# Performance work log

Measured on AMD Instinct MI355X. Metric: run time of the kernel, lower is better.

The kernel has to match this reference:

```python
import jax, jax.numpy as jnp
import numpy as np

NUM_HEADS = 32
NUM_KV_HEADS = 8
HEAD_DIM = 128
ROPE_BASE = 10000.0


def rotate_half(x):
    half = x.shape[-1] // 2
    x1, x2 = x[..., :half], x[..., half:]
    return jnp.concatenate((-x2, x1), axis=-1)


def rope_cos_sin(position_ids, head_dim, dtype):
    # inv_freq: [head_dim/2]
    inv_freq = 1.0 / (ROPE_BASE ** (jnp.arange(0, head_dim, 2, dtype=jnp.float32) / head_dim))
    freqs = position_ids.astype(jnp.float32)[..., None] * inv_freq  # [B, S, hd/2]
    emb = jnp.concatenate((freqs, freqs), axis=-1)                  # [B, S, hd]
    # add head axis -> [B, 1, S, hd]
    return jnp.cos(emb)[:, None].astype(dtype), jnp.sin(emb)[:, None].astype(dtype)


def setup_inputs() -> dict:
    key = jax.random.key(0)
    k_x, k_q, k_k, k_v, k_o = jax.random.split(key, 5)
    B, S, H = 1, 2048, 4096
    w_scale = 0.02
    return {
        "hidden_states": jax.random.normal(k_x, (B, S, H), dtype=jnp.float32),
        "position_ids": jnp.broadcast_to(jnp.arange(S, dtype=jnp.int32), (B, S)),
        "Wq": jax.random.normal(k_q, (NUM_HEADS * HEAD_DIM, H), dtype=jnp.float32) * w_scale,
        "Wk": jax.random.normal(k_k, (NUM_KV_HEADS * HEAD_DIM, H), dtype=jnp.float32) * w_scale,
        "Wv": jax.random.normal(k_v, (NUM_KV_HEADS * HEAD_DIM, H), dtype=jnp.float32) * w_scale,
        "Wo": jax.random.normal(k_o, (H, NUM_HEADS * HEAD_DIM), dtype=jnp.float32) * w_scale,
    }


def reference(hidden_states, position_ids, Wq, Wk, Wv, Wo):
    B, S, H = hidden_states.shape
    n_rep = NUM_HEADS // NUM_KV_HEADS

    # projections (torch Linear: y = x @ W.T), reshape to [B, heads, S, hd]
    q = (hidden_states @ Wq.T).reshape(B, S, NUM_HEADS, HEAD_DIM).transpose(0, 2, 1, 3)
    k = (hidden_states @ Wk.T).reshape(B, S, NUM_KV_HEADS, HEAD_DIM).transpose(0, 2, 1, 3)
    v = (hidden_states @ Wv.T).reshape(B, S, NUM_KV_HEADS, HEAD_DIM).transpose(0, 2, 1, 3)

    cos, sin = rope_cos_sin(position_ids, HEAD_DIM, hidden_states.dtype)
    q = q * cos + rotate_half(q) * sin
    k = k * cos + rotate_half(k) * sin

    # repeat_kv: GQA expansion to [B, NUM_HEADS, S, hd]
    k = jnp.repeat(k, n_rep, axis=1)
    v = jnp.repeat(v, n_rep, axis=1)

    scale = 1.0 / jnp.sqrt(jnp.asarray(HEAD_DIM, dtype=hidden_states.dtype))
    scores = jnp.einsum('bhqd,bhkd->bhqk', q, k) * scale  # [B, H, S, S]

    # causal additive mask
    causal = jnp.tril(jnp.ones((S, S), dtype=bool))
    scores = jnp.where(causal[None, None], scores, jnp.finfo(scores.dtype).min)

    probs = jax.nn.softmax(scores, axis=-1)
    attn = jnp.einsum('bhqk,bhkd->bhqd', probs, v)         # [B, H, S, hd]
    attn = attn.transpose(0, 2, 1, 3).reshape(B, S, NUM_HEADS * HEAD_DIM)
    return attn @ Wo.T
```

## Files before the change

kernel.cpp:

```cpp
#include <hip/hip_runtime.h>
#include <hip/hip_bf16.h>
#include <stdint.h>

typedef __bf16 bf16;
typedef __attribute__((ext_vector_type(8))) __bf16 bf16x8;
typedef __attribute__((ext_vector_type(4))) __bf16 bf16x4;
typedef __attribute__((ext_vector_type(4))) float f32x4;
typedef __attribute__((ext_vector_type(16))) float f32x16;
typedef __attribute__((ext_vector_type(4))) unsigned int uint4v;

#define S_LEN 2048
#define HDIM  4096
#define NQH   32
#define NKVH  8
#define DHEAD 128
#define QKVN  6144
#define KOFF  4096
#define VOFF  5120

__device__ __forceinline__ void gload_lds16(const bf16* g, bf16* l) {
  __builtin_amdgcn_global_load_lds(
      (const __attribute__((address_space(1))) unsigned int*)g,
      (__attribute__((address_space(3))) unsigned int*)l, 16, 0, 0);
}

__global__ __launch_bounds__(256) void cvt_f32_bf16(const float* __restrict__ in,
                                                    bf16* __restrict__ out, int n4) {
  int i = blockIdx.x * 256 + threadIdx.x;
  if (i >= n4) return;
  float4 v = ((const float4*)in)[i];
  bf16x4 ov = {(bf16)v.x, (bf16)v.y, (bf16)v.z, (bf16)v.w};
  *(bf16x4*)&out[(size_t)i * 4] = ov;
}

__global__ __launch_bounds__(256) void rope_table(const int* __restrict__ pos,
                                                  float* __restrict__ tab) {
  int idx = blockIdx.x * 256 + threadIdx.x;
  int i = idx & 63, s = idx >> 6;
  float p = (float)pos[s];
  float invf = powf(10000.0f, -(float)i * (1.0f / 64.0f));
  float ang = p * invf;
  tab[idx * 2]     = cosf(ang);
  tab[idx * 2 + 1] = sinf(ang);
}

__global__ __launch_bounds__(256) void rope_apply(bf16* __restrict__ QKV,
                                                  const float* __restrict__ tab) {
  int idx = blockIdx.x * 256 + threadIdx.x;
  int dp = idx & 63;
  int t = idx >> 6;
  int head = t % 40;
  int s = t / 40;
  float c  = tab[(s * 64 + dp) * 2];
  float sn = tab[(s * 64 + dp) * 2 + 1];
  size_t base = (size_t)s * QKVN + head * DHEAD;
  float x0 = (float)QKV[base + dp];
  float x1 = (float)QKV[base + 64 + dp];
  QKV[base + dp]      = (bf16)(x0 * c - x1 * sn);
  QKV[base + 64 + dp] = (bf16)(x1 * c + x0 * sn);
}

__global__ __launch_bounds__(256) void transpose_v(const bf16* __restrict__ QKV,
                                                   bf16* __restrict__ Vt) {
  __shared__ bf16 t[64][72];
  int tid = threadIdx.x;
  int bs = blockIdx.x * 64, bc = blockIdx.y * 64;
  int sl = tid >> 3, cb = (tid & 7) * 8;
#pragma unroll
  for (int ss = 0; ss < 64; ss += 32) {
    int s = sl + ss;
    *(bf16x8*)&t[s][cb] = *(const bf16x8*)&QKV[(size_t)(bs + s) * QKVN + VOFF + bc + cb];
  }
  __syncthreads();
  int cl = tid >> 3, sb = (tid & 7) * 8;
#pragma unroll
  for (int cc = 0; cc < 64; cc += 32) {
    int c = cl + cc;
    bf16x8 v;
#pragma unroll
    for (int k = 0; k < 8; ++k) v[k] = t[sb + k][c];
    *(bf16x8*)&Vt[(size_t)(bc + c) * S_LEN + bs + sb] = v;
  }
}

template <typename OutT>
__global__ __launch_bounds__(256) void gemm_bt(const bf16* __restrict__ A,
                                               const bf16* __restrict__ B,
                                               OutT* __restrict__ C,
                                               int M, int N, int K) {
  __shared__ bf16 At[128 * 64];
  __shared__ bf16 Bt[128 * 64];
  const int tid = threadIdx.x;
  const int w = tid >> 6, lane = tid & 63;
  const int r = lane & 15, g = lane >> 4;
  const int bm = blockIdx.y * 128, bn = blockIdx.x * 128;
  const int wm = (w >> 1) * 64, wn = (w & 1) * 64;
  f32x4 acc[4][4];
#pragma unroll
  for (int i = 0; i < 4; ++i)
#pragma unroll
    for (int j = 0; j < 4; ++j) acc[i][j] = (f32x4){0.f, 0.f, 0.f, 0.f};

  const int chunk0 = w * 256 + lane;

  for (int k0 = 0; k0 < K; k0 += 64) {
#pragma unroll
    for (int i = 0; i < 4; ++i) {
      int chunk = chunk0 + i * 64;
      int row = chunk >> 3, c8 = chunk & 7;
      int cs = ((c8 ^ (row & 7)) << 3) + k0;
      gload_lds16(&A[(size_t)(bm + row) * K + cs], &At[(w * 4 + i) * 512]);
      gload_lds16(&B[(size_t)(bn + row) * K + cs], &Bt[(w * 4 + i) * 512]);
    }
    __syncthreads();
#pragma unroll
    for (int ks = 0; ks < 2; ++ks) {
      bf16x8 af[4], bfr[4];
#pragma unroll
      for (int mi = 0; mi < 4; ++mi) {
        int row = wm + mi * 16 + r;
        af[mi] = *(const bf16x8*)&At[row * 64 + ((((ks << 2) + g) ^ (row & 7)) << 3)];
      }
#pragma unroll
      for (int nj = 0; nj < 4; ++nj) {
        int row = wn + nj * 16 + r;
        bfr[nj] = *(const bf16x8*)&Bt[row * 64 + ((((ks << 2) + g) ^ (row & 7)) << 3)];
      }
#pragma unroll
      for (int mi = 0; mi < 4; ++mi)
#pragma unroll
        for (int nj = 0; nj < 4; ++nj)
          acc[mi][nj] = __builtin_amdgcn_mfma_f32_16x16x32_bf16(af[mi], bfr[nj],
                                                                acc[mi][nj], 0, 0, 0);
    }
    __syncthreads();
  }
#pragma unroll
  for (int mi = 0; mi < 4; ++mi)
#pragma unroll
    for (int nj = 0; nj < 4; ++nj)
#pragma unroll
      for (int j = 0; j < 4; ++j) {
        int row = bm + wm + mi * 16 + g * 4 + j;
        int col = bn + wn + nj * 16 + r;
        C[(size_t)row * N + col] = (OutT)acc[mi][nj][j];
      }
}

__global__ __launch_bounds__(256) void attn_kernel(const bf16* __restrict__ QKV,
                                                   const bf16* __restrict__ Vt,
                                                   bf16* __restrict__ Opart,
                                                   float* __restrict__ Mpart,
                                                   float* __restrict__ Lpart) {
  __shared__ bf16 Kl[2][32 * 128];
  __shared__ bf16 Vl[2][128 * 32];
  const int tid = threadIdx.x;
  const int w = tid >> 6, lane = tid & 63;
  const int l31 = lane & 31, hi = lane >> 5;
  const int bx = blockIdx.x;
  const int kvh = bx & 7;
  const int rem = bx >> 3;
  const int s = rem & 1;
  const int u = rem >> 1;
  const int ua = u & 15, ub = u >> 4;
  const int qblk = (ub & 1) ? ((3 - ub) * 16 + (15 - ua)) : ((3 - ub) * 16 + ua);
  const int h = kvh * 4 + w;
  const int q0 = qblk * 32;
  const int pid = (h * 64 + qblk) * 2 + s;
  const float scale = 0.12751746f;

  const int nt = qblk + 1;
  const int hh = (nt + 1) >> 1;
  const int t0 = s ? hh : 0;
  const int t1 = s ? nt : hh;

  f32x16 o[4];
#pragma unroll
  for (int t = 0; t < 4; ++t)
#pragma unroll
    for (int r = 0; r < 16; ++r) o[t][r] = 0.f;
  float m_run = -1e30f, l_run = 0.f;

  auto stage = [&](int bufi, int kv0) {
#pragma unroll
    for (int ii = 0; ii < 2; ++ii) {
      int ins = w * 2 + ii;
      int kr = ins * 4 + (lane >> 4);
      int ck = (lane & 15) ^ (kr & 15);
      gload_lds16(&QKV[(size_t)(kv0 + kr) * QKVN + KOFF + kvh * DHEAD + ck * 8],
                  &Kl[bufi][ins * 512]);
      int d = ins * 16 + (lane >> 2);
      int cv = (lane & 3) ^ (d & 3);
      gload_lds16(&Vt[(size_t)(kvh * DHEAD + d) * S_LEN + kv0 + cv * 8],
                  &Vl[bufi][ins * 512]);
    }
  };

  if (t0 < t1) {
    bf16x8 qf[8];
#pragma unroll
    for (int k8 = 0; k8 < 8; ++k8) {
      bf16x8 raw = *(const bf16x8*)&QKV[(size_t)(q0 + l31) * QKVN + h * DHEAD + k8 * 16 + hi * 8];
#pragma unroll
      for (int e = 0; e < 8; ++e) qf[k8][e] = (bf16)((float)raw[e] * scale);
    }

    stage(t0 & 1, t0 * 32);
    __syncthreads();

    for (int t = t0; t < t1; ++t) {
      const int cur = t & 1;
      if (t + 1 < t1) stage(cur ^ 1, (t + 1) * 32);

      f32x16 st;
#pragma unroll
      for (int r = 0; r < 16; ++r) st[r] = 0.f;
      __builtin_amdgcn_s_setprio(1);
#pragma unroll
      for (int k8 = 0; k8 < 8; ++k8) {
        bf16x8 kf = *(const bf16x8*)&Kl[cur][l31 * 128 +
                                            (((2 * k8 + hi) ^ (l31 & 15)) << 3)];
        st = __builtin_amdgcn_mfma_f32_32x32x16_bf16(kf, qf[k8], st, 0, 0, 0);
      }
      __builtin_amdgcn_s_setprio(0);

      if (t == nt - 1) {
#pragma unroll
        for (int r = 0; r < 16; ++r) {
          int kvr = (r & 3) + 8 * (r >> 2) + 4 * hi;
          if (kvr > l31) st[r] = -1e30f;
        }
      }
      float pmax = st[0];
#pragma unroll
      for (int r = 1; r < 16; ++r) pmax = fmaxf(pmax, st[r]);
      pmax = fmaxf(pmax, __shfl_xor(pmax, 32));
      if (!__all(pmax - m_run <= 8.0f)) {
        float mnew = fmaxf(m_run, pmax);
        float corr = exp2f(m_run - mnew);
        m_run = mnew;
        l_run *= corr;
#pragma unroll
        for (int r = 0; r < 16; ++r) {
          float cr = __shfl(corr, (r & 3) + 8 * (r >> 2) + 4 * hi);
          o[0][r] *= cr; o[1][r] *= cr; o[2][r] *= cr; o[3][r] *= cr;
        }
      }
      float p[16], rs = 0.f;
#pragma unroll
      for (int r = 0; r < 16; ++r) { p[r] = exp2f(st[r] - m_run); rs += p[r]; }
      rs += __shfl_xor(rs, 32);
      l_run += rs;
      unsigned int A[8], X[8];
#pragma unroll
      for (int j = 0; j < 8; ++j) {
        unsigned short lo = __builtin_bit_cast(unsigned short, (bf16)p[2 * j]);
        unsigned short hi16 = __builtin_bit_cast(unsigned short, (bf16)p[2 * j + 1]);
        A[j] = (unsigned int)lo | ((unsigned int)hi16 << 16);
      }
#pragma unroll
      for (int j = 0; j < 8; ++j) X[j] = __shfl_xor(A[j], 32);
      uint4v w0v = {hi ? X[2] : A[0], hi ? X[3] : A[1],
                    hi ? A[2] : X[0], hi ? A[3] : X[1]};
      uint4v w1v = {hi ? X[6] : A[4], hi ? X[7] : A[5],
                    hi ? A[6] : X[4], hi ? A[7] : X[5]};
      bf16x8 pf0 = __builtin_bit_cast(bf16x8, w0v);
      bf16x8 pf1 = __builtin_bit_cast(bf16x8, w1v);
      __builtin_amdgcn_s_setprio(1);
#pragma unroll
      for (int tt = 0; tt < 4; ++tt) {
        int dt = tt * 32 + l31;
        bf16x8 v0 = *(const bf16x8*)&Vl[cur][dt * 32 + ((hi ^ (l31 & 3)) << 3)];
        bf16x8 v1 = *(const bf16x8*)&Vl[cur][dt * 32 + (((2 + hi) ^ (l31 & 3)) << 3)];
        o[tt] = __builtin_amdgcn_mfma_f32_32x32x16_bf16(pf0, v0, o[tt], 0, 0, 0);
        o[tt] = __builtin_amdgcn_mfma_f32_32x32x16_bf16(pf1, v1, o[tt], 0, 0, 0);
      }
      __builtin_amdgcn_s_setprio(0);
      __syncthreads();
    }
  }

  float linv = (l_run > 0.f) ? 1.0f / l_run : 0.f;
  if (hi == 0) {
    Mpart[pid * 32 + l31] = m_run;
    Lpart[pid * 32 + l31] = l_run;
  }
#pragma unroll
  for (int r = 0; r < 16; ++r) {
    int qloc = (r & 3) + 8 * (r >> 2) + 4 * hi;
    float li = __shfl(linv, qloc);
    size_t row = (size_t)pid * (32 * DHEAD) + (size_t)qloc * DHEAD;
#pragma unroll
    for (int t2 = 0; t2 < 4; ++t2)
      Opart[row + t2 * 32 + l31] = (bf16)(o[t2][r] * li);
  }
}

__global__ __launch_bounds__(256) void attn_merge(const bf16* __restrict__ Opart,
                                                  const float* __restrict__ Mpart,
                                                  const float* __restrict__ Lpart,
                                                  bf16* __restrict__ Oout) {
  const int bx = blockIdx.x;
  const int h = bx >> 6, qblk = bx & 63;
  const int tid = threadIdx.x;
  const int r = tid >> 3, cseg = (tid & 7) * 16;
  const int pid0 = bx * 2, pid1 = pid0 + 1;
  float m0 = Mpart[pid0 * 32 + r], m1 = Mpart[pid1 * 32 + r];
  float l0 = Lpart[pid0 * 32 + r], l1 = Lpart[pid1 * 32 + r];
  float M = fmaxf(m0, m1);
  float w0 = l0 * exp2f(m0 - M), w1 = l1 * exp2f(m1 - M);
  float inv = 1.0f / (w0 + w1);
  w0 *= inv; w1 *= inv;
  size_t src0 = (size_t)pid0 * (32 * DHEAD) + (size_t)r * DHEAD + cseg;
  size_t src1 = (size_t)pid1 * (32 * DHEAD) + (size_t)r * DHEAD + cseg;
  size_t dst = (size_t)(qblk * 32 + r) * HDIM + h * DHEAD + cseg;
#pragma unroll
  for (int half = 0; half < 2; ++half) {
    bf16x8 a = *(const bf16x8*)&Opart[src0 + half * 8];
    bf16x8 b = *(const bf16x8*)&Opart[src1 + half * 8];
    bf16x8 out;
#pragma unroll
    for (int e = 0; e < 8; ++e) out[e] = (bf16)(w0 * (float)a[e] + w1 * (float)b[e]);
    *(bf16x8*)&Oout[dst + half * 8] = out;
  }
}

extern "C" void kernel_launch(void* const* d_in, const int* in_sizes, int n_in,
                              void* d_out, int out_size, void* d_ws, size_t ws_size,
                              hipStream_t stream) {
  const float* X   = (const float*)d_in[0];
  const int*   pos = (const int*)d_in[1];
  const float* Wq  = (const float*)d_in[2];
  const float* Wk  = (const float*)d_in[3];
  const float* Wv  = (const float*)d_in[4];
  const float* Wo  = (const float*)d_in[5];
  float* out = (float*)d_out;
  char* ws = (char*)d_ws;

  size_t off = 0;
  bf16* Xb    = (bf16*)(ws + off); off += (size_t)2048 * 4096 * 2;
  bf16* Wqkvb = (bf16*)(ws + off); off += (size_t)6144 * 4096 * 2;
  bf16* Wob   = (bf16*)(ws + off); off += (size_t)4096 * 4096 * 2;
  bf16* QKV   = (bf16*)(ws + off); off += (size_t)2048 * 6144 * 2;
  bf16* Vt    = (bf16*)(ws + off); off += (size_t)1024 * 2048 * 2;
  bf16* attnb = (bf16*)(ws + off); off += (size_t)2048 * 4096 * 2;
  float* tab  = (float*)(ws + off); off += (size_t)2048 * 64 * 2 * 4;

  bf16*  Opart = (bf16*)Wqkvb;
  float* Mpart = (float*)((char*)Wqkvb + (size_t)4096 * 32 * 128 * 2);
  float* Lpart = Mpart + (size_t)4096 * 32;

  cvt_f32_bf16<<<2048 * 4096 / 4 / 256, 256, 0, stream>>>(X, Xb, 2048 * 4096 / 4);
  cvt_f32_bf16<<<4096 * 4096 / 4 / 256, 256, 0, stream>>>(Wq, Wqkvb, 4096 * 4096 / 4);
  cvt_f32_bf16<<<1024 * 4096 / 4 / 256, 256, 0, stream>>>(Wk, Wqkvb + (size_t)4096 * 4096,
                                                          1024 * 4096 / 4);
  cvt_f32_bf16<<<1024 * 4096 / 4 / 256, 256, 0, stream>>>(Wv, Wqkvb + (size_t)5120 * 4096,
                                                          1024 * 4096 / 4);
  cvt_f32_bf16<<<4096 * 4096 / 4 / 256, 256, 0, stream>>>(Wo, Wob, 4096 * 4096 / 4);
  rope_table<<<2048 * 64 / 256, 256, 0, stream>>>(pos, tab);
  gemm_bt<bf16><<<dim3(QKVN / 128, 2048 / 128), 256, 0, stream>>>(Xb, Wqkvb, QKV,
                                                                  2048, QKVN, 4096);
  rope_apply<<<2048 * 40 * 64 / 256, 256, 0, stream>>>(QKV, tab);
  transpose_v<<<dim3(2048 / 64, 1024 / 64), 256, 0, stream>>>(QKV, Vt);
  attn_kernel<<<1024, 256, 0, stream>>>(QKV, Vt, Opart, Mpart, Lpart);
  attn_merge<<<2048, 256, 0, stream>>>(Opart, Mpart, Lpart, attnb);
  gemm_bt<float><<<dim3(4096 / 128, 2048 / 128), 256, 0, stream>>>(attnb, Wob, out,
                                                                   2048, 4096, 4096);
}
```

Before: 400.0 us.

## Split attention KV range four ways and rework LDS swizzles

Raises the flash-decoding style split of each query block's KV range from 2 to 4 partitions, doubling attention grid size, and orders blocks largest-qblk-first instead of the old zigzag. K and V LDS layouts get new XOR swizzles over 8-chunk groups. The P packing is also restructured to reuse the score registers. The merge kernel now combines four partials, and the partial buffers move to Xb plus fresh workspace. More merge traffic and tiny splits for early query blocks are the costs.

```diff
diff --git a/kernel.cpp b/kernel.cpp
--- a/kernel.cpp
+++ b/kernel.cpp
@@ -17,6 +17,7 @@
 #define QKVN  6144
 #define KOFF  4096
 #define VOFF  5120
+#define NSPLIT 4
 
 __device__ __forceinline__ void gload_lds16(const bf16* g, bf16* l) {
   __builtin_amdgcn_global_load_lds(
@@ -159,20 +160,17 @@
   const int l31 = lane & 31, hi = lane >> 5;
   const int bx = blockIdx.x;
   const int kvh = bx & 7;
-  const int rem = bx >> 3;
-  const int s = rem & 1;
-  const int u = rem >> 1;
-  const int ua = u & 15, ub = u >> 4;
-  const int qblk = (ub & 1) ? ((3 - ub) * 16 + (15 - ua)) : ((3 - ub) * 16 + ua);
+  const int rest = bx >> 3;
+  const int s = rest & 3;
+  const int qblk = 63 - (rest >> 2);
   const int h = kvh * 4 + w;
   const int q0 = qblk * 32;
-  const int pid = (h * 64 + qblk) * 2 + s;
+  const int pid = (h * 64 + qblk) * NSPLIT + s;
   const float scale = 0.12751746f;
 
   const int nt = qblk + 1;
-  const int hh = (nt + 1) >> 1;
-  const int t0 = s ? hh : 0;
-  const int t1 = s ? nt : hh;
+  const int t0 = (nt * s) >> 2;
+  const int t1 = (nt * (s + 1)) >> 2;
 
   f32x16 o[4];
 #pragma unroll
@@ -185,13 +183,15 @@
 #pragma unroll
     for (int ii = 0; ii < 2; ++ii) {
       int ins = w * 2 + ii;
-      int kr = ins * 4 + (lane >> 4);
-      int ck = (lane & 15) ^ (kr & 15);
-      gload_lds16(&QKV[(size_t)(kv0 + kr) * QKVN + KOFF + kvh * DHEAD + ck * 8],
+      int hr = ins * 8 + (lane >> 3);
+      int kvrow = hr >> 1, hK = hr & 1;
+      int gk = ((lane & 7) ^ (kvrow & 7)) + 8 * hK;
+      gload_lds16(&QKV[(size_t)(kv0 + kvrow) * QKVN + KOFF + kvh * DHEAD + gk * 8],
                   &Kl[bufi][ins * 512]);
-      int d = ins * 16 + (lane >> 2);
-      int cv = (lane & 3) ^ (d & 3);
-      gload_lds16(&Vt[(size_t)(kvh * DHEAD + d) * S_LEN + kv0 + cv * 8],
+      int pr = ins * 8 + (lane >> 3);
+      int xv = (lane & 7) ^ (pr & 7);
+      int dV = pr * 2 + (xv >> 2);
+      gload_lds16(&Vt[(size_t)(kvh * DHEAD + dV) * S_LEN + kv0 + (xv & 3) * 8],
                   &Vl[bufi][ins * 512]);
     }
   };
@@ -218,8 +218,9 @@
       __builtin_amdgcn_s_setprio(1);
 #pragma unroll
       for (int k8 = 0; k8 < 8; ++k8) {
-        bf16x8 kf = *(const bf16x8*)&Kl[cur][l31 * 128 +
-                                            (((2 * k8 + hi) ^ (l31 & 15)) << 3)];
+        int g = 2 * k8 + hi;
+        bf16x8 kf = *(const bf16x8*)&Kl[cur][l31 * 128 + (g >> 3) * 64 +
+                                             (((g & 7) ^ (l31 & 7)) << 3)];
         st = __builtin_amdgcn_mfma_f32_32x32x16_bf16(kf, qf[k8], st, 0, 0, 0);
       }
       __builtin_amdgcn_s_setprio(0);
@@ -246,32 +247,47 @@
           o[0][r] *= cr; o[1][r] *= cr; o[2][r] *= cr; o[3][r] *= cr;
         }
       }
-      float p[16], rs = 0.f;
-#pragma unroll
-      for (int r = 0; r < 16; ++r) { p[r] = exp2f(st[r] - m_run); rs += p[r]; }
+      float rs = 0.f;
+#pragma unroll
+      for (int r = 0; r < 16; ++r) { st[r] = exp2f(st[r] - m_run); rs += st[r]; }
       rs += __shfl_xor(rs, 32);
       l_run += rs;
-      unsigned int A[8], X[8];
-#pragma unroll
-      for (int j = 0; j < 8; ++j) {
-        unsigned short lo = __builtin_bit_cast(unsigned short, (bf16)p[2 * j]);
-        unsigned short hi16 = __builtin_bit_cast(unsigned short, (bf16)p[2 * j + 1]);
-        A[j] = (unsigned int)lo | ((unsigned int)hi16 << 16);
-      }
-#pragma unroll
-      for (int j = 0; j < 8; ++j) X[j] = __shfl_xor(A[j], 32);
-      uint4v w0v = {hi ? X[2] : A[0], hi ? X[3] : A[1],
-                    hi ? A[2] : X[0], hi ? A[3] : X[1]};
-      uint4v w1v = {hi ? X[6] : A[4], hi ? X[7] : A[5],
-                    hi ? A[6] : X[4], hi ? A[7] : X[5]};
-      bf16x8 pf0 = __builtin_bit_cast(bf16x8, w0v);
-      bf16x8 pf1 = __builtin_bit_cast(bf16x8, w1v);
+      bf16x8 pf0, pf1;
+      {
+        unsigned int A0[4], X0[4];
+#pragma unroll
+        for (int j = 0; j < 4; ++j) {
+          unsigned short lo = __builtin_bit_cast(unsigned short, (bf16)st[2 * j]);
+          unsigned short hi16 = __builtin_bit_cast(unsigned short, (bf16)st[2 * j + 1]);
+          A0[j] = (unsigned int)lo | ((unsigned int)hi16 << 16);
+        }
+#pragma unroll
+        for (int j = 0; j < 4; ++j) X0[j] = __shfl_xor(A0[j], 32);
+        uint4v w0v = {hi ? X0[2] : A0[0], hi ? X0[3] : A0[1],
+                      hi ? A0[2] : X0[0], hi ? A0[3] : X0[1]};
+        pf0 = __builtin_bit_cast(bf16x8, w0v);
+      }
+      {
+        unsigned int A1[4], X1[4];
+#pragma unroll
+        for (int j = 0; j < 4; ++j) {
+          unsigned short lo = __builtin_bit_cast(unsigned short, (bf16)st[8 + 2 * j]);
+          unsigned short hi16 = __builtin_bit_cast(unsigned short, (bf16)st[9 + 2 * j]);
+          A1[j] = (unsigned int)lo | ((unsigned int)hi16 << 16);
+        }
+#pragma unroll
+        for (int j = 0; j < 4; ++j) X1[j] = __shfl_xor(A1[j], 32);
+        uint4v w1v = {hi ? X1[2] : A1[0], hi ? X1[3] : A1[1],
+                      hi ? A1[2] : X1[0], hi ? A1[3] : X1[1]};
+        pf1 = __builtin_bit_cast(bf16x8, w1v);
+      }
       __builtin_amdgcn_s_setprio(1);
 #pragma unroll
       for (int tt = 0; tt < 4; ++tt) {
-        int dt = tt * 32 + l31;
-        bf16x8 v0 = *(const bf16x8*)&Vl[cur][dt * 32 + ((hi ^ (l31 & 3)) << 3)];
-        bf16x8 v1 = *(const bf16x8*)&Vl[cur][dt * 32 + (((2 + hi) ^ (l31 & 3)) << 3)];
+        int pr = tt * 16 + (l31 >> 1);
+        int sb4 = (l31 & 1) << 2;
+        bf16x8 v0 = *(const bf16x8*)&Vl[cur][pr * 64 + (((sb4 + hi) ^ (pr & 7)) << 3)];
+        bf16x8 v1 = *(const bf16x8*)&Vl[cur][pr * 64 + (((sb4 + 2 + hi) ^ (pr & 7)) << 3)];
         o[tt] = __builtin_amdgcn_mfma_f32_32x32x16_bf16(pf0, v0, o[tt], 0, 0, 0);
         o[tt] = __builtin_amdgcn_mfma_f32_32x32x16_bf16(pf1, v1, o[tt], 0, 0, 0);
       }
@@ -304,23 +320,37 @@
   const int h = bx >> 6, qblk = bx & 63;
   const int tid = threadIdx.x;
   const int r = tid >> 3, cseg = (tid & 7) * 16;
-  const int pid0 = bx * 2, pid1 = pid0 + 1;
-  float m0 = Mpart[pid0 * 32 + r], m1 = Mpart[pid1 * 32 + r];
-  float l0 = Lpart[pid0 * 32 + r], l1 = Lpart[pid1 * 32 + r];
-  float M = fmaxf(m0, m1);
-  float w0 = l0 * exp2f(m0 - M), w1 = l1 * exp2f(m1 - M);
-  float inv = 1.0f / (w0 + w1);
-  w0 *= inv; w1 *= inv;
-  size_t src0 = (size_t)pid0 * (32 * DHEAD) + (size_t)r * DHEAD + cseg;
-  size_t src1 = (size_t)pid1 * (32 * DHEAD) + (size_t)r * DHEAD + cseg;
+  const int pid0 = bx * NSPLIT;
+  float m[NSPLIT], l[NSPLIT];
+  float M = -1e30f;
+#pragma unroll
+  for (int s = 0; s < NSPLIT; ++s) {
+    m[s] = Mpart[(pid0 + s) * 32 + r];
+    l[s] = Lpart[(pid0 + s) * 32 + r];
+    M = fmaxf(M, m[s]);
+  }
+  float wsum = 0.f, wv[NSPLIT];
+#pragma unroll
+  for (int s = 0; s < NSPLIT; ++s) { wv[s] = l[s] * exp2f(m[s] - M); wsum += wv[s]; }
+  float inv = 1.0f / wsum;
+#pragma unroll
+  for (int s = 0; s < NSPLIT; ++s) wv[s] *= inv;
   size_t dst = (size_t)(qblk * 32 + r) * HDIM + h * DHEAD + cseg;
 #pragma unroll
   for (int half = 0; half < 2; ++half) {
-    bf16x8 a = *(const bf16x8*)&Opart[src0 + half * 8];
-    bf16x8 b = *(const bf16x8*)&Opart[src1 + half * 8];
+    float acc[8];
+#pragma unroll
+    for (int e = 0; e < 8; ++e) acc[e] = 0.f;
+#pragma unroll
+    for (int s = 0; s < NSPLIT; ++s) {
+      bf16x8 a = *(const bf16x8*)&Opart[(size_t)(pid0 + s) * (32 * DHEAD) +
+                                        (size_t)r * DHEAD + cseg + half * 8];
+#pragma unroll
+      for (int e = 0; e < 8; ++e) acc[e] += wv[s] * (float)a[e];
+    }
     bf16x8 out;
 #pragma unroll
-    for (int e = 0; e < 8; ++e) out[e] = (bf16)(w0 * (float)a[e] + w1 * (float)b[e]);
+    for (int e = 0; e < 8; ++e) out[e] = (bf16)acc[e];
     *(bf16x8*)&Oout[dst + half * 8] = out;
   }
 }
@@ -345,10 +375,10 @@
   bf16* Vt    = (bf16*)(ws + off); off += (size_t)1024 * 2048 * 2;
   bf16* attnb = (bf16*)(ws + off); off += (size_t)2048 * 4096 * 2;
   float* tab  = (float*)(ws + off); off += (size_t)2048 * 64 * 2 * 4;
-
-  bf16*  Opart = (bf16*)Wqkvb;
-  float* Mpart = (float*)((char*)Wqkvb + (size_t)4096 * 32 * 128 * 2);
-  float* Lpart = Mpart + (size_t)4096 * 32;
+  float* Mpart = (float*)(ws + off); off += (size_t)8192 * 32 * 4;
+  float* Lpart = (float*)(ws + off); off += (size_t)8192 * 32 * 4;
+
+  bf16* Opart = (bf16*)Xb;
 
   cvt_f32_bf16<<<2048 * 4096 / 4 / 256, 256, 0, stream>>>(X, Xb, 2048 * 4096 / 4);
   cvt_f32_bf16<<<4096 * 4096 / 4 / 256, 256, 0, stream>>>(Wq, Wqkvb, 4096 * 4096 / 4);
@@ -362,7 +392,7 @@
                                                                   2048, QKVN, 4096);
   rope_apply<<<2048 * 40 * 64 / 256, 256, 0, stream>>>(QKV, tab);
   transpose_v<<<dim3(2048 / 64, 1024 / 64), 256, 0, stream>>>(QKV, Vt);
-  attn_kernel<<<1024, 256, 0, stream>>>(QKV, Vt, Opart, Mpart, Lpart);
+  attn_kernel<<<2048, 256, 0, stream>>>(QKV, Vt, Opart, Mpart, Lpart);
   attn_merge<<<2048, 256, 0, stream>>>(Opart, Mpart, Lpart, attnb);
   gemm_bt<float><<<dim3(4096 / 128, 2048 / 128), 256, 0, stream>>>(attnb, Wob, out,
                                                                    2048, 4096, 4096);
```

Result: slower. 415.3 us (+3.8%).
